# Kernel tuning notes

Measured on AMD Instinct MI355X. Metric: run time of the kernel, lower is better.

## Reference

```python
import jax, jax.numpy as jnp
import numpy as np

NUME = 30000; NUMR = 8; DIM_IN = 128; DIM_OUT = 128; DIM_R = 64; DIM_T = 32
DEEPTH = 2; HEADS = 4; DHEAD = DIM_OUT // HEADS; R_TOTAL = 2 * NUMR + 1  # r0..r7, -r0..-r7, self
N_NODES = 20000; N_EDGES = 15000; BATCH = 1024; T_MAX = 32; DIN = DIM_IN + DIM_T
NEG_SLOPE = 0.2  # DGL GATConv default leaky_relu slope


def setup_inputs() -> dict:
    key = jax.random.key(0)
    ks = jax.random.split(key, 16)
    inp = {}
    inp['node_ids'] = jax.random.randint(ks[0], (N_NODES,), 0, NUME * T_MAX)
    inp['edge_src'] = jax.random.randint(ks[1], (R_TOTAL, N_EDGES), 0, N_NODES)
    inp['edge_dst'] = jax.random.randint(ks[2], (R_TOTAL, N_EDGES), 0, N_NODES)
    inp['root_idx'] = jax.random.randint(ks[3], (2 * BATCH,), 0, N_NODES)
    inp['rel'] = jax.random.randint(ks[4], (BATCH,), 0, NUMR)
    inp['entity_emb'] = jax.random.normal(ks[5], (NUME, DIM_IN), jnp.float32) * 0.02
    inp['basis_freq'] = jnp.asarray(1.0 / 10 ** np.linspace(0, 9, DIM_T), dtype=jnp.float32)
    inp['phase'] = jnp.zeros((DIM_T,), jnp.float32)
    inp['fc_w'] = jax.random.normal(ks[6], (DEEPTH, R_TOTAL, DIN, DIM_OUT), jnp.float32) / np.float32(np.sqrt(DIN))
    inp['attn_l'] = jax.random.normal(ks[7], (DEEPTH, R_TOTAL, HEADS, DHEAD), jnp.float32) * 0.1
    inp['attn_r'] = jax.random.normal(ks[8], (DEEPTH, R_TOTAL, HEADS, DHEAD), jnp.float32) * 0.1
    inp['sub_rel_emb'] = jax.random.normal(ks[9], (NUMR, DIM_R), jnp.float32) * 0.02
    inp['obj_rel_emb'] = jax.random.normal(ks[10], (NUMR, DIM_R), jnp.float32) * 0.02
    inp['sub_cls_w'] = jax.random.normal(ks[11], (DIM_OUT + DIM_R, NUME), jnp.float32) / np.float32(np.sqrt(DIM_OUT + DIM_R))
    inp['sub_cls_b'] = jnp.zeros((NUME,), jnp.float32)
    inp['obj_cls_w'] = jax.random.normal(ks[12], (DIM_OUT + DIM_R, NUME), jnp.float32) / np.float32(np.sqrt(DIM_OUT + DIM_R))
    inp['obj_cls_b'] = jnp.zeros((NUME,), jnp.float32)
    inp['ts'] = 31
    return inp


def gat_relation(feat, src, dst, w, a_l, a_r):
    # DGL GATConv: feat [N, DIN], src/dst [E], w [DIN, H*Dh], a_l/a_r [H, Dh]
    z = (feat @ w).reshape(N_NODES, HEADS, DHEAD)          # fc projection
    el = jnp.einsum('nhd,hd->nh', z, a_l)                  # src attention term
    er = jnp.einsum('nhd,hd->nh', z, a_r)                  # dst attention term
    e = el[src] + er[dst]                                  # [E, H]
    e = jnp.where(e >= 0, e, NEG_SLOPE * e)                # leaky_relu
    m = jax.ops.segment_max(e, dst, num_segments=N_NODES)  # edge-softmax per dst
    m = jnp.where(jnp.isfinite(m), m, 0.0)                 # empty segments -> 0
    ex = jnp.exp(e - m[dst])
    den = jax.ops.segment_sum(ex, dst, num_segments=N_NODES)
    alpha = ex / jnp.maximum(den[dst], 1e-9)
    msg = alpha[:, :, None] * z[src]                       # [E, H, Dh]
    return jax.ops.segment_sum(msg, dst, num_segments=N_NODES)  # [N, H, Dh]


def reference(node_ids, edge_src, edge_dst, root_idx, rel, entity_emb, basis_freq,
              phase, fc_w, attn_l, attn_r, sub_rel_emb, obj_rel_emb,
              sub_cls_w, sub_cls_b, obj_cls_w, obj_cls_b, ts):
    t_s = ts - 1  # source does ts -= 1
    h = entity_emb[jnp.remainder(node_ids, NUME)]          # entity_emb lookup
    # TimeEnc: cos((ts - nid // nume) * freq + phase); block node set identical per layer here
    dt = (t_s - node_ids // NUME).astype(jnp.float32)
    phi = jnp.cos(dt[:, None] * basis_freq + phase)        # [N, DIM_T]
    for l in range(DEEPTH):
        x = jnp.concatenate([h, phi], axis=1)              # [N, DIN]
        # HeteroGraphConv: one GATConv per relation type, vmapped over R_TOTAL
        outs = jax.vmap(lambda s, d, w, al, ar: gat_relation(x, s, d, w, al, ar))(
            edge_src, edge_dst, fc_w[l], attn_l[l], attn_r[l])  # [R, N, H, Dh]
        h = outs.mean(axis=0).reshape(N_NODES, DIM_OUT)    # aggregate='mean', then flatten heads
        h = jax.nn.relu(h)                                 # act (dropout is identity in eval)
    emb = h[root_idx]                                      # [2B, DIM_OUT]
    sub_emb = emb[:BATCH]
    obj_emb = emb[BATCH:]
    sub_pred = jnp.concatenate([obj_emb, obj_rel_emb[rel]], axis=1) @ sub_cls_w + sub_cls_b
    obj_pred = jnp.concatenate([sub_emb, sub_rel_emb[rel]], axis=1) @ obj_cls_w + obj_cls_b
    return sub_pred, obj_pred
```

## Files before the change

### kernel.cpp

```cpp
#include <hip/hip_runtime.h>
#include <hip/hip_bf16.h>
#include <math.h>

#define NUME 30000
#define DIM_IN 128
#define DIM_OUT 128
#define DIM_R 64
#define DIM_T 32
#define HEADS 4
#define DHEAD 32
#define R_TOTAL 17
#define N_NODES 20000
#define N_EDGES 15000
#define DIN 160
#define NEG_SLOPE 0.2f
#define ECOLS 136

__device__ __forceinline__ unsigned fkey(float f){
  unsigned u = __float_as_uint(f);
  return (u & 0x80000000u) ? ~u : (u | 0x80000000u);
}
__device__ __forceinline__ float funkey(unsigned k){
  unsigned u = (k & 0x80000000u) ? (k & 0x7FFFFFFFu) : ~k;
  return __uint_as_float(u);
}
#define MKEY_NEG_INF 0x007FFFFFu

__global__ __launch_bounds__(256) void k_build_x(const int* node_ids, const float* entity_emb,
                                                 const float* basis_freq, const float* phase,
                                                 const int* ts_p, float* x){
  int i = blockIdx.x * 256 + threadIdx.x;
  if (i >= N_NODES * DIN) return;
  int n = i / DIN, c = i % DIN;
  int nid = node_ids[n];
  if (c < DIM_IN){
    x[i] = entity_emb[(size_t)(nid % NUME) * DIM_IN + c];
  } else {
    int t = c - DIM_IN;
    float dt = (float)(ts_p[0] - 1 - nid / NUME);
    x[i] = cosf(dt * basis_freq[t] + phase[t]);
  }
}

__global__ __launch_bounds__(256) void k_wa(const float* fc_w, const float* attn_l,
                                            const float* attn_r, float* wa){
  int lr = blockIdx.x;
  int l = lr / R_TOTAL, r = lr % R_TOTAL;
  const float* w  = fc_w  + (size_t)lr * DIN * DIM_OUT;
  const float* al = attn_l + (size_t)lr * HEADS * DHEAD;
  const float* ar = attn_r + (size_t)lr * HEADS * DHEAD;
  for (int i = threadIdx.x; i < DIN * HEADS; i += 256){
    int k = i / HEADS, h = i % HEADS;
    float sl = 0.f, sr = 0.f;
    for (int d = 0; d < DHEAD; ++d){
      float wv = w[(size_t)k * DIM_OUT + h * DHEAD + d];
      sl += wv * al[h * DHEAD + d];
      sr += wv * ar[h * DHEAD + d];
    }
    wa[((size_t)l * DIN + k) * ECOLS + r * 8 + h]     = sl;
    wa[((size_t)l * DIN + k) * ECOLS + r * 8 + 4 + h] = sr;
  }
}

__global__ __launch_bounds__(256) void k_layer_init(float* h_acc, unsigned* mkey, float* den){
  int i = blockIdx.x * 256 + threadIdx.x;
  if (i < N_NODES * DIM_OUT) h_acc[i] = 0.f;
  if (i < R_TOTAL * N_NODES * HEADS){ mkey[i] = MKEY_NEG_INF; den[i] = 0.f; }
}

__global__ __launch_bounds__(256) void k_elr(const float* x, const float* wa, float* elr, int l){
  __shared__ float sX[64][33];
  __shared__ float sWA[32][ECOLS];
  int n0 = blockIdx.x * 64;
  int tid = threadIdx.x;
  int nt = tid & 31, ct = tid >> 5;
  float acc[2][17] = {};
  for (int kc = 0; kc < 5; ++kc){
    __syncthreads();
    for (int i = tid; i < 64 * 32; i += 256){
      int nn = i >> 5, kk = i & 31;
      int n = n0 + nn;
      sX[nn][kk] = (n < N_NODES) ? x[(size_t)n * DIN + kc * 32 + kk] : 0.f;
    }
    for (int i = tid; i < 32 * ECOLS; i += 256){
      int kk = i / ECOLS, c = i % ECOLS;
      sWA[kk][c] = wa[((size_t)l * DIN + kc * 32 + kk) * ECOLS + c];
    }
    __syncthreads();
    for (int kk = 0; kk < 32; ++kk){
      float x0 = sX[nt][kk], x1 = sX[nt + 32][kk];
      #pragma unroll
      for (int j = 0; j < 17; ++j){
        float wv = sWA[kk][ct * 17 + j];
        acc[0][j] += x0 * wv;
        acc[1][j] += x1 * wv;
      }
    }
  }
  #pragma unroll
  for (int q = 0; q < 2; ++q){
    int n = n0 + nt + q * 32;
    if (n < N_NODES)
      for (int j = 0; j < 17; ++j)
        elr[(size_t)n * ECOLS + ct * 17 + j] = acc[q][j];
  }
}

__global__ __launch_bounds__(256) void k_edge1(const int* edge_src, const int* edge_dst,
                                               const float* elr, float* e_edge, unsigned* mkey){
  int i = blockIdx.x * 256 + threadIdx.x;
  if (i >= R_TOTAL * N_EDGES) return;
  int r = i / N_EDGES;
  int s = edge_src[i], d = edge_dst[i];
  const float* el = &elr[(size_t)s * ECOLS + r * 8];
  const float* er = &elr[(size_t)d * ECOLS + r * 8 + 4];
  #pragma unroll
  for (int h = 0; h < 4; ++h){
    float v = el[h] + er[h];
    v = v >= 0.f ? v : NEG_SLOPE * v;
    e_edge[(size_t)i * 4 + h] = v;
    atomicMax(&mkey[((size_t)r * N_NODES + d) * 4 + h], fkey(v));
  }
}

__global__ __launch_bounds__(256) void k_edge2(const int* edge_dst, const float* e_edge,
                                               const unsigned* mkey, float* ex_edge, float* den){
  int i = blockIdx.x * 256 + threadIdx.x;
  if (i >= R_TOTAL * N_EDGES) return;
  int r = i / N_EDGES;
  int d = edge_dst[i];
  #pragma unroll
  for (int h = 0; h < 4; ++h){
    float m = funkey(mkey[((size_t)r * N_NODES + d) * 4 + h]);
    float ex = expf(e_edge[(size_t)i * 4 + h] - m);
    ex_edge[(size_t)i * 4 + h] = ex;
    atomicAdd(&den[((size_t)r * N_NODES + d) * 4 + h], ex);
  }
}

#define EB 64
__global__ __launch_bounds__(256) void k_msg(const int* edge_src, const int* edge_dst,
                                             const float* x, const float* fc_w,
                                             const float* ex_edge, const float* den,
                                             float* h_acc, int l){
  __shared__ float sX[EB][161];
  __shared__ float sW[32][128];
  __shared__ float sAl[EB][4];
  __shared__ int sSrc[EB], sDst[EB];
  int r = blockIdx.y;
  int e0 = blockIdx.x * EB;
  int tid = threadIdx.x;

  if (tid < EB){
    int e = e0 + tid;
    int s = 0, d = 0;
    if (e < N_EDGES){
      s = edge_src[(size_t)r * N_EDGES + e];
      d = edge_dst[(size_t)r * N_EDGES + e];
    }
    sSrc[tid] = s; sDst[tid] = d;
  }
  {
    int e = e0 + (tid >> 2), h = tid & 3;
    float a = 0.f;
    if (e < N_EDGES){
      int d = edge_dst[(size_t)r * N_EDGES + e];
      a = ex_edge[((size_t)r * N_EDGES + e) * 4 + h] /
          fmaxf(den[((size_t)r * N_NODES + d) * 4 + h], 1e-9f);
    }
    sAl[tid >> 2][h] = a;
  }
  __syncthreads();
  for (int i = tid; i < EB * DIN; i += 256){
    int e = i / DIN, k = i % DIN;
    sX[e][k] = x[(size_t)sSrc[e] * DIN + k];
  }

  const float* w = fc_w + ((size_t)(l * R_TOTAL + r)) * DIN * DIM_OUT;
  int eg = tid >> 4;
  int cg = tid & 15;
  float acc[4][8] = {};
  for (int kc = 0; kc < 5; ++kc){
    __syncthreads();
    for (int i = tid; i < 32 * 32; i += 256){
      int kk = i >> 5, c4 = i & 31;
      *(float4*)&sW[kk][c4 * 4] = *(const float4*)&w[(size_t)(kc * 32 + kk) * DIM_OUT + c4 * 4];
    }
    __syncthreads();
    for (int kk = 0; kk < 32; ++kk){
      float4 w0 = *(float4*)&sW[kk][cg * 8];
      float4 w1 = *(float4*)&sW[kk][cg * 8 + 4];
      #pragma unroll
      for (int i2 = 0; i2 < 4; ++i2){
        float xv = sX[eg * 4 + i2][kc * 32 + kk];
        acc[i2][0] += xv * w0.x; acc[i2][1] += xv * w0.y;
        acc[i2][2] += xv * w0.z; acc[i2][3] += xv * w0.w;
        acc[i2][4] += xv * w1.x; acc[i2][5] += xv * w1.y;
        acc[i2][6] += xv * w1.z; acc[i2][7] += xv * w1.w;
      }
    }
  }
  #pragma unroll
  for (int i2 = 0; i2 < 4; ++i2){
    int e = eg * 4 + i2;
    if (e0 + e < N_EDGES){
      int d = sDst[e];
      float a = sAl[e][cg >> 2];
      #pragma unroll
      for (int j = 0; j < 8; ++j)
        atomicAdd(&h_acc[(size_t)d * DIM_OUT + cg * 8 + j], a * acc[i2][j]);
    }
  }
}

__global__ __launch_bounds__(256) void k_mean(const float* h_acc, float* x){
  int i = blockIdx.x * 256 + threadIdx.x;
  if (i >= N_NODES * DIM_OUT) return;
  int n = i >> 7, c = i & 127;
  float v = h_acc[i] * (1.0f / 17.0f);
  x[(size_t)n * DIN + c] = fmaxf(v, 0.f);
}

__global__ __launch_bounds__(256) void k_cat(const int* root_idx, const int* rel, const float* x,
                                             const float* sub_rel_emb, const float* obj_rel_emb,
                                             float* A){
  int i = blockIdx.x * 256 + threadIdx.x;
  if (i >= 2048 * 192) return;
  int row = i / 192, k = i % 192;
  int b = row & 1023;
  bool top = row < 1024;
  float v;
  if (k < 128){
    int node = root_idx[top ? (1024 + b) : b];
    v = x[(size_t)node * DIN + k];
  } else {
    const float* re = top ? obj_rel_emb : sub_rel_emb;
    v = re[(size_t)rel[b] * DIM_R + (k - 128)];
  }
  A[i] = v;
}

__global__ __launch_bounds__(256) void k_cls(const float* A, const float* w_sub, const float* b_sub,
                                             const float* w_obj, const float* b_obj, float* out){
  __shared__ float sA[64][33];
  __shared__ float sW[32][128];
  int rb = blockIdx.y, cb = blockIdx.x;
  int row0 = rb * 64, col0 = cb * 128;
  const float* w    = (rb < 16) ? w_sub : w_obj;
  const float* bias = (rb < 16) ? b_sub : b_obj;
  int tid = threadIdx.x;
  int tr = tid >> 5, tc = tid & 31;
  float acc[8][4] = {};
  for (int kc = 0; kc < 6; ++kc){
    __syncthreads();
    for (int i = tid; i < 64 * 32; i += 256){
      int rr = i >> 5, kk = i & 31;
      sA[rr][kk] = A[(size_t)(row0 + rr) * 192 + kc * 32 + kk];
    }
    for (int i = tid; i < 32 * 32; i += 256){
      int kk = i >> 5, c4 = i & 31;
      int col = col0 + c4 * 4;
      float4 v = make_float4(0.f, 0.f, 0.f, 0.f);
      if (col < 30000) v = *(const float4*)&w[(size_t)(kc * 32 + kk) * 30000 + col];
      *(float4*)&sW[kk][c4 * 4] = v;
    }
    __syncthreads();
    for (int kk = 0; kk < 32; ++kk){
      float4 wv = *(float4*)&sW[kk][tc * 4];
      #pragma unroll
      for (int i2 = 0; i2 < 8; ++i2){
        float av = sA[tr * 8 + i2][kk];
        acc[i2][0] += av * wv.x; acc[i2][1] += av * wv.y;
        acc[i2][2] += av * wv.z; acc[i2][3] += av * wv.w;
      }
    }
  }
  int col = col0 + tc * 4;
  if (col < 30000){
    float4 bv = *(const float4*)&bias[col];
    #pragma unroll
    for (int i2 = 0; i2 < 8; ++i2){
      int row = row0 + tr * 8 + i2;
      float4 o = make_float4(acc[i2][0] + bv.x, acc[i2][1] + bv.y,
                             acc[i2][2] + bv.z, acc[i2][3] + bv.w);
      *(float4*)&out[(size_t)row * 30000 + col] = o;
    }
  }
}

extern "C" void kernel_launch(void* const* d_in, const int* in_sizes, int n_in,
                              void* d_out, int out_size, void* d_ws, size_t ws_size,
                              hipStream_t stream){
  const int*   node_ids    = (const int*)  d_in[0];
  const int*   edge_src    = (const int*)  d_in[1];
  const int*   edge_dst    = (const int*)  d_in[2];
  const int*   root_idx    = (const int*)  d_in[3];
  const int*   rel         = (const int*)  d_in[4];
  const float* entity_emb  = (const float*)d_in[5];
  const float* basis_freq  = (const float*)d_in[6];
  const float* phase       = (const float*)d_in[7];
  const float* fc_w        = (const float*)d_in[8];
  const float* attn_l      = (const float*)d_in[9];
  const float* attn_r      = (const float*)d_in[10];
  const float* sub_rel_emb = (const float*)d_in[11];
  const float* obj_rel_emb = (const float*)d_in[12];
  const float* sub_cls_w   = (const float*)d_in[13];
  const float* sub_cls_b   = (const float*)d_in[14];
  const float* obj_cls_w   = (const float*)d_in[15];
  const float* obj_cls_b   = (const float*)d_in[16];
  const int*   ts_p        = (const int*)  d_in[17];
  float* out = (float*)d_out;

  char* p = (char*)d_ws;
  auto alloc = [&](size_t bytes) -> char* {
    char* q = p; p += (bytes + 255) & ~(size_t)255; return q;
  };
  float*    x       = (float*)   alloc((size_t)N_NODES * DIN * 4);
  float*    elr     = (float*)   alloc((size_t)N_NODES * ECOLS * 4);
  unsigned* mkey    = (unsigned*)alloc((size_t)R_TOTAL * N_NODES * HEADS * 4);
  float*    den     = (float*)   alloc((size_t)R_TOTAL * N_NODES * HEADS * 4);
  float*    e_edge  = (float*)   alloc((size_t)R_TOTAL * N_EDGES * HEADS * 4);
  float*    ex_edge = (float*)   alloc((size_t)R_TOTAL * N_EDGES * HEADS * 4);
  float*    h_acc   = (float*)   alloc((size_t)N_NODES * DIM_OUT * 4);
  float*    wa      = (float*)   alloc((size_t)2 * DIN * ECOLS * 4);
  float*    A_cat   = (float*)   alloc((size_t)2048 * 192 * 4);

  k_wa<<<2 * R_TOTAL, 256, 0, stream>>>(fc_w, attn_l, attn_r, wa);
  k_build_x<<<(N_NODES * DIN + 255) / 256, 256, 0, stream>>>(node_ids, entity_emb, basis_freq,
                                                             phase, ts_p, x);
  for (int l = 0; l < 2; ++l){
    k_layer_init<<<(N_NODES * DIM_OUT + 255) / 256, 256, 0, stream>>>(h_acc, mkey, den);
    k_elr<<<(N_NODES + 63) / 64, 256, 0, stream>>>(x, wa, elr, l);
    k_edge1<<<(R_TOTAL * N_EDGES + 255) / 256, 256, 0, stream>>>(edge_src, edge_dst, elr,
                                                                 e_edge, mkey);
    k_edge2<<<(R_TOTAL * N_EDGES + 255) / 256, 256, 0, stream>>>(edge_dst, e_edge, mkey,
                                                                 ex_edge, den);
    k_msg<<<dim3((N_EDGES + EB - 1) / EB, R_TOTAL), 256, 0, stream>>>(edge_src, edge_dst, x,
                                                                      fc_w, ex_edge, den,
                                                                      h_acc, l);
    k_mean<<<(N_NODES * DIM_OUT + 255) / 256, 256, 0, stream>>>(h_acc, x);
  }
  k_cat<<<(2048 * 192 + 255) / 256, 256, 0, stream>>>(root_idx, rel, x,
                                                      sub_rel_emb, obj_rel_emb, A_cat);
  k_cls<<<dim3((30000 + 127) / 128, 32), 256, 0, stream>>>(A_cat, sub_cls_w, sub_cls_b,
                                                           obj_cls_w, obj_cls_b, out);
}
```

Before: 18.46 ms.

## Replace atomic scatter with CSR-by-destination gather for softmax and aggregation

Builds a per-(relation, dst) CSR edge index once with count, scan and fill kernels. Edge softmax and message aggregation then run as per-destination gathers instead of atomicMax, atomicAdd and float atomic scatter into h_acc. Messages are stored per edge as bf16 and summed in k_gather, which also applies the mean and relu. This removes atomic contention and the init and mean kernels, but adds a single-block scan, a large bf16 message buffer, and some precision loss.

Measured after the change: 19.09 ms. +3.4%, slower.

```diff
diff --git a/kernel.cpp b/kernel.cpp
--- a/kernel.cpp
+++ b/kernel.cpp
@@ -1,5 +1,4 @@
 #include <hip/hip_runtime.h>
-#include <hip/hip_bf16.h>
 #include <math.h>
 
 #define NUME 30000
@@ -15,16 +14,18 @@
 #define DIN 160
 #define NEG_SLOPE 0.2f
 #define ECOLS 136
-
-__device__ __forceinline__ unsigned fkey(float f){
+#define NKEY (R_TOTAL * N_NODES)
+#define NE_ALL (R_TOTAL * N_EDGES)
+
+typedef __attribute__((ext_vector_type(8))) unsigned short ushort8;
+
+__device__ __forceinline__ unsigned short f2bf(float f){
   unsigned u = __float_as_uint(f);
-  return (u & 0x80000000u) ? ~u : (u | 0x80000000u);
-}
-__device__ __forceinline__ float funkey(unsigned k){
-  unsigned u = (k & 0x80000000u) ? (k & 0x7FFFFFFFu) : ~k;
-  return __uint_as_float(u);
-}
-#define MKEY_NEG_INF 0x007FFFFFu
+  return (unsigned short)((u + 0x7FFFu + ((u >> 16) & 1u)) >> 16);
+}
+__device__ __forceinline__ float bf2f(unsigned short b){
+  return __uint_as_float((unsigned)b << 16);
+}
 
 __global__ __launch_bounds__(256) void k_build_x(const int* node_ids, const float* entity_emb,
                                                  const float* basis_freq, const float* phase,
@@ -62,10 +63,52 @@
   }
 }
 
-__global__ __launch_bounds__(256) void k_layer_init(float* h_acc, unsigned* mkey, float* den){
-  int i = blockIdx.x * 256 + threadIdx.x;
-  if (i < N_NODES * DIM_OUT) h_acc[i] = 0.f;
-  if (i < R_TOTAL * N_NODES * HEADS){ mkey[i] = MKEY_NEG_INF; den[i] = 0.f; }
+__global__ __launch_bounds__(256) void k_zero_count(int* count){
+  int i = blockIdx.x * 256 + threadIdx.x;
+  if (i < NKEY) count[i] = 0;
+}
+__global__ __launch_bounds__(256) void k_count(const int* edge_dst, int* count){
+  int i = blockIdx.x * 256 + threadIdx.x;
+  if (i >= NE_ALL) return;
+  int r = i / N_EDGES;
+  atomicAdd(&count[r * N_NODES + edge_dst[i]], 1);
+}
+__global__ __launch_bounds__(1024) void k_scan(const int* count, int* row_start){
+  __shared__ int part[1024];
+  int t = threadIdx.x;
+  const int CH = (NKEY + 1023) / 1024;
+  int base = t * CH;
+  int s = 0;
+  for (int i = 0; i < CH; ++i){
+    int idx = base + i;
+    if (idx < NKEY) s += count[idx];
+  }
+  part[t] = s;
+  __syncthreads();
+  for (int off = 1; off < 1024; off <<= 1){
+    int v = (t >= off) ? part[t - off] : 0;
+    __syncthreads();
+    part[t] += v;
+    __syncthreads();
+  }
+  int excl = (t == 0) ? 0 : part[t - 1];
+  for (int i = 0; i < CH; ++i){
+    int idx = base + i;
+    if (idx <= NKEY) row_start[idx] = excl;
+    if (idx < NKEY) excl += count[idx];
+  }
+}
+__global__ __launch_bounds__(256) void k_copy_cursor(const int* row_start, int* cursor){
+  int i = blockIdx.x * 256 + threadIdx.x;
+  if (i < NKEY) cursor[i] = row_start[i];
+}
+__global__ __launch_bounds__(256) void k_fill(const int* edge_dst, int* cursor, int* eidlist){
+  int i = blockIdx.x * 256 + threadIdx.x;
+  if (i >= NE_ALL) return;
+  int r = i / N_EDGES;
+  int key = r * N_NODES + edge_dst[i];
+  int pos = atomicAdd(&cursor[key], 1);
+  eidlist[pos] = i;
 }
 
 __global__ __launch_bounds__(256) void k_elr(const float* x, const float* wa, float* elr, int l){
@@ -106,10 +149,10 @@
   }
 }
 
-__global__ __launch_bounds__(256) void k_edge1(const int* edge_src, const int* edge_dst,
-                                               const float* elr, float* e_edge, unsigned* mkey){
-  int i = blockIdx.x * 256 + threadIdx.x;
-  if (i >= R_TOTAL * N_EDGES) return;
+__global__ __launch_bounds__(256) void k_edge_e(const int* edge_src, const int* edge_dst,
+                                                const float* elr, float* e_edge){
+  int i = blockIdx.x * 256 + threadIdx.x;
+  if (i >= NE_ALL) return;
   int r = i / N_EDGES;
   int s = edge_src[i], d = edge_dst[i];
   const float* el = &elr[(size_t)s * ECOLS + r * 8];
@@ -119,55 +162,51 @@
     float v = el[h] + er[h];
     v = v >= 0.f ? v : NEG_SLOPE * v;
     e_edge[(size_t)i * 4 + h] = v;
-    atomicMax(&mkey[((size_t)r * N_NODES + d) * 4 + h], fkey(v));
-  }
-}
-
-__global__ __launch_bounds__(256) void k_edge2(const int* edge_dst, const float* e_edge,
-                                               const unsigned* mkey, float* ex_edge, float* den){
-  int i = blockIdx.x * 256 + threadIdx.x;
-  if (i >= R_TOTAL * N_EDGES) return;
-  int r = i / N_EDGES;
-  int d = edge_dst[i];
-  #pragma unroll
-  for (int h = 0; h < 4; ++h){
-    float m = funkey(mkey[((size_t)r * N_NODES + d) * 4 + h]);
-    float ex = expf(e_edge[(size_t)i * 4 + h] - m);
-    ex_edge[(size_t)i * 4 + h] = ex;
-    atomicAdd(&den[((size_t)r * N_NODES + d) * 4 + h], ex);
-  }
+  }
+}
+
+__global__ __launch_bounds__(256) void k_soft(const int* row_start, const int* eidlist,
+                                              const float* e_edge, float* alpha){
+  int i = blockIdx.x * 256 + threadIdx.x;
+  if (i >= NKEY * HEADS) return;
+  int key = i >> 2, h = i & 3;
+  int b = row_start[key], e = row_start[key + 1];
+  if (b == e) return;
+  float m = -INFINITY;
+  for (int idx = b; idx < e; ++idx)
+    m = fmaxf(m, e_edge[(size_t)eidlist[idx] * 4 + h]);
+  float den = 0.f;
+  for (int idx = b; idx < e; ++idx){
+    float ex = expf(e_edge[(size_t)eidlist[idx] * 4 + h] - m);
+    alpha[(size_t)eidlist[idx] * 4 + h] = ex;
+    den += ex;
+  }
+  float inv = 1.f / fmaxf(den, 1e-9f);
+  for (int idx = b; idx < e; ++idx)
+    alpha[(size_t)eidlist[idx] * 4 + h] *= inv;
 }
 
 #define EB 64
-__global__ __launch_bounds__(256) void k_msg(const int* edge_src, const int* edge_dst,
-                                             const float* x, const float* fc_w,
-                                             const float* ex_edge, const float* den,
-                                             float* h_acc, int l){
+__global__ __launch_bounds__(256) void k_msg(const int* edge_src, const float* x,
+                                             const float* fc_w, const float* alpha,
+                                             unsigned short* msg, int l){
   __shared__ float sX[EB][161];
   __shared__ float sW[32][128];
   __shared__ float sAl[EB][4];
-  __shared__ int sSrc[EB], sDst[EB];
+  __shared__ int sSrc[EB];
   int r = blockIdx.y;
   int e0 = blockIdx.x * EB;
   int tid = threadIdx.x;
 
   if (tid < EB){
     int e = e0 + tid;
-    int s = 0, d = 0;
-    if (e < N_EDGES){
-      s = edge_src[(size_t)r * N_EDGES + e];
-      d = edge_dst[(size_t)r * N_EDGES + e];
-    }
-    sSrc[tid] = s; sDst[tid] = d;
+    sSrc[tid] = (e < N_EDGES) ? edge_src[(size_t)r * N_EDGES + e] : 0;
   }
   {
     int e = e0 + (tid >> 2), h = tid & 3;
     float a = 0.f;
-    if (e < N_EDGES){
-      int d = edge_dst[(size_t)r * N_EDGES + e];
-      a = ex_edge[((size_t)r * N_EDGES + e) * 4 + h] /
-          fmaxf(den[((size_t)r * N_NODES + d) * 4 + h], 1e-9f);
-    }
+    if (e < N_EDGES)
+      a = alpha[((size_t)r * N_EDGES + e) * 4 + h];
     sAl[tid >> 2][h] = a;
   }
   __syncthreads();
@@ -204,21 +243,30 @@
   for (int i2 = 0; i2 < 4; ++i2){
     int e = eg * 4 + i2;
     if (e0 + e < N_EDGES){
-      int d = sDst[e];
       float a = sAl[e][cg >> 2];
+      ushort8 v;
       #pragma unroll
       for (int j = 0; j < 8; ++j)
-        atomicAdd(&h_acc[(size_t)d * DIM_OUT + cg * 8 + j], a * acc[i2][j]);
-    }
-  }
-}
-
-__global__ __launch_bounds__(256) void k_mean(const float* h_acc, float* x){
-  int i = blockIdx.x * 256 + threadIdx.x;
-  if (i >= N_NODES * DIM_OUT) return;
-  int n = i >> 7, c = i & 127;
-  float v = h_acc[i] * (1.0f / 17.0f);
-  x[(size_t)n * DIN + c] = fmaxf(v, 0.f);
+        v[j] = f2bf(a * acc[i2][j]);
+      *(ushort8*)&msg[((size_t)r * N_EDGES + e0 + e) * DIM_OUT + cg * 8] = v;
+    }
+  }
+}
+
+__global__ __launch_bounds__(256) void k_gather(const int* row_start, const int* eidlist,
+                                                const unsigned short* msg, float* x){
+  int tid = threadIdx.x;
+  int n = blockIdx.x * 2 + (tid >> 7);
+  int c = tid & 127;
+  if (n >= N_NODES) return;
+  float acc = 0.f;
+  for (int r = 0; r < R_TOTAL; ++r){
+    int key = r * N_NODES + n;
+    int b = row_start[key], e = row_start[key + 1];
+    for (int idx = b; idx < e; ++idx)
+      acc += bf2f(msg[(size_t)eidlist[idx] * DIM_OUT + c]);
+  }
+  x[(size_t)n * DIN + c] = fmaxf(acc * (1.0f / 17.0f), 0.f);
 }
 
 __global__ __launch_bounds__(256) void k_cat(const int* root_idx, const int* rel, const float* x,
@@ -315,30 +363,34 @@
   auto alloc = [&](size_t bytes) -> char* {
     char* q = p; p += (bytes + 255) & ~(size_t)255; return q;
   };
-  float*    x       = (float*)   alloc((size_t)N_NODES * DIN * 4);
-  float*    elr     = (float*)   alloc((size_t)N_NODES * ECOLS * 4);
-  unsigned* mkey    = (unsigned*)alloc((size_t)R_TOTAL * N_NODES * HEADS * 4);
-  float*    den     = (float*)   alloc((size_t)R_TOTAL * N_NODES * HEADS * 4);
-  float*    e_edge  = (float*)   alloc((size_t)R_TOTAL * N_EDGES * HEADS * 4);
-  float*    ex_edge = (float*)   alloc((size_t)R_TOTAL * N_EDGES * HEADS * 4);
-  float*    h_acc   = (float*)   alloc((size_t)N_NODES * DIM_OUT * 4);
-  float*    wa      = (float*)   alloc((size_t)2 * DIN * ECOLS * 4);
-  float*    A_cat   = (float*)   alloc((size_t)2048 * 192 * 4);
+  float*    x        = (float*)   alloc((size_t)N_NODES * DIN * 4);
+  float*    elr      = (float*)   alloc((size_t)N_NODES * ECOLS * 4);
+  float*    e_edge   = (float*)   alloc((size_t)NE_ALL * HEADS * 4);
+  float*    alpha    = (float*)   alloc((size_t)NE_ALL * HEADS * 4);
+  int*      count    = (int*)     alloc((size_t)NKEY * 4);
+  int*      row_start= (int*)     alloc((size_t)(NKEY + 1) * 4);
+  int*      cursor   = (int*)     alloc((size_t)NKEY * 4);
+  int*      eidlist  = (int*)     alloc((size_t)NE_ALL * 4);
+  float*    wa       = (float*)   alloc((size_t)2 * DIN * ECOLS * 4);
+  float*    A_cat    = (float*)   alloc((size_t)2048 * 192 * 4);
+  unsigned short* msg = (unsigned short*)alloc((size_t)NE_ALL * DIM_OUT * 2);
+
+  k_zero_count<<<(NKEY + 255) / 256, 256, 0, stream>>>(count);
+  k_count<<<(NE_ALL + 255) / 256, 256, 0, stream>>>(edge_dst, count);
+  k_scan<<<1, 1024, 0, stream>>>(count, row_start);
+  k_copy_cursor<<<(NKEY + 255) / 256, 256, 0, stream>>>(row_start, cursor);
+  k_fill<<<(NE_ALL + 255) / 256, 256, 0, stream>>>(edge_dst, cursor, eidlist);
 
   k_wa<<<2 * R_TOTAL, 256, 0, stream>>>(fc_w, attn_l, attn_r, wa);
   k_build_x<<<(N_NODES * DIN + 255) / 256, 256, 0, stream>>>(node_ids, entity_emb, basis_freq,
                                                              phase, ts_p, x);
   for (int l = 0; l < 2; ++l){
-    k_layer_init<<<(N_NODES * DIM_OUT + 255) / 256, 256, 0, stream>>>(h_acc, mkey, den);
     k_elr<<<(N_NODES + 63) / 64, 256, 0, stream>>>(x, wa, elr, l);
-    k_edge1<<<(R_TOTAL * N_EDGES + 255) / 256, 256, 0, stream>>>(edge_src, edge_dst, elr,
-                                                                 e_edge, mkey);
-    k_edge2<<<(R_TOTAL * N_EDGES + 255) / 256, 256, 0, stream>>>(edge_dst, e_edge, mkey,
-                                                                 ex_edge, den);
-    k_msg<<<dim3((N_EDGES + EB - 1) / EB, R_TOTAL), 256, 0, stream>>>(edge_src, edge_dst, x,
-                                                                      fc_w, ex_edge, den,
-                                                                      h_acc, l);
-    k_mean<<<(N_NODES * DIM_OUT + 255) / 256, 256, 0, stream>>>(h_acc, x);
+    k_edge_e<<<(NE_ALL + 255) / 256, 256, 0, stream>>>(edge_src, edge_dst, elr, e_edge);
+    k_soft<<<(NKEY * HEADS + 255) / 256, 256, 0, stream>>>(row_start, eidlist, e_edge, alpha);
+    k_msg<<<dim3((N_EDGES + EB - 1) / EB, R_TOTAL), 256, 0, stream>>>(edge_src, x, fc_w,
+                                                                      alpha, msg, l);
+    k_gather<<<(N_NODES + 1) / 2, 256, 0, stream>>>(row_start, eidlist, msg, x);
   }
   k_cat<<<(2048 * 192 + 255) / 256, 256, 0, stream>>>(root_idx, rel, x,
                                                       sub_rel_emb, obj_rel_emb, A_cat);
```
